# Kernel optimization log

Measured on AMD Instinct MI355X. Metric: run time of the kernel, lower is better.

The kernel has to match this reference:

```python
import jax, jax.numpy as jnp
import numpy as np

START, STOP, T = 28, 29, 30

def _lstm_dir(x, h0, c0, w_ih, w_hh, b_ih, b_hh):
    # x: (S, B, E) -> hs: (S, B, H)
    xw = jnp.einsum('sbe,ge->sbg', x, w_ih) + b_ih + b_hh  # (S,B,4H)
    def step(carry, g_x):
        h, c = carry
        g = g_x + h @ w_hh.T
        i, f, gg, o = jnp.split(g, 4, axis=-1)
        c = jax.nn.sigmoid(f) * c + jax.nn.sigmoid(i) * jnp.tanh(gg)
        h = jax.nn.sigmoid(o) * jnp.tanh(c)
        return (h, c), h
    _, hs = jax.lax.scan(step, (h0, c0), xw)
    return hs

def setup_inputs() -> dict:
    key = jax.random.key(0)
    ks = jax.random.split(key, 16)
    S, B, V, E, H = 256, 32, 50000, 512, 512  # H = hidden_dim // 2
    d = {}
    d['sentence'] = jax.random.randint(ks[0], (S, B), 0, V)
    d['tags'] = jax.random.randint(ks[1], (S, B), 0, 28)
    d['emb'] = jax.random.normal(ks[2], (V, E), jnp.float32) * 0.1
    d['w_ih_f'] = jax.random.normal(ks[3], (4 * H, E), jnp.float32) * 0.05
    d['w_hh_f'] = jax.random.normal(ks[4], (4 * H, H), jnp.float32) * 0.05
    d['b_ih_f'] = jax.random.normal(ks[5], (4 * H,), jnp.float32) * 0.05
    d['b_hh_f'] = jax.random.normal(ks[6], (4 * H,), jnp.float32) * 0.05
    d['w_ih_b'] = jax.random.normal(ks[7], (4 * H, E), jnp.float32) * 0.05
    d['w_hh_b'] = jax.random.normal(ks[8], (4 * H, H), jnp.float32) * 0.05
    d['b_ih_b'] = jax.random.normal(ks[9], (4 * H,), jnp.float32) * 0.05
    d['b_hh_b'] = jax.random.normal(ks[10], (4 * H,), jnp.float32) * 0.05
    d['w_out'] = jax.random.normal(ks[11], (T, 2 * H), jnp.float32) * 0.05
    d['b_out'] = jax.random.normal(ks[12], (T,), jnp.float32) * 0.05
    tr = jax.random.normal(ks[13], (T, T), jnp.float32)
    tr = tr.at[START, :].set(-10000.0).at[:, STOP].set(-10000.0)
    d['transitions'] = tr
    d['h0'] = jax.random.normal(ks[14], (2, B, H), jnp.float32)
    d['c0'] = jax.random.normal(ks[15], (2, B, H), jnp.float32)
    return d

def reference(sentence, tags, emb, w_ih_f, w_hh_f, b_ih_f, b_hh_f,
              w_ih_b, w_hh_b, b_ih_b, b_hh_b, w_out, b_out, transitions, h0, c0):
    S, B = sentence.shape
    x = emb[sentence]                                   # (S,B,E)
    hf = _lstm_dir(x, h0[0], c0[0], w_ih_f, w_hh_f, b_ih_f, b_hh_f)
    hb = _lstm_dir(x[::-1], h0[1], c0[1], w_ih_b, w_hh_b, b_ih_b, b_hh_b)[::-1]
    lstm_out = jnp.concatenate([hf, hb], axis=-1)       # (S,B,2H)
    feats = jnp.einsum('sbh,th->bst', lstm_out, w_out) + b_out  # (B,S,T)

    # CRF partition function (forward algorithm)
    fv0 = jnp.full((B, T), -10000.0, feats.dtype).at[:, START].set(0.0)
    def crf_step(fv, feat):  # fv (B,T), feat (B,T)
        fv = jax.nn.logsumexp(fv[:, None, :] + transitions[None, :, :] + feat[:, :, None], axis=2)
        return fv, None
    fv, _ = jax.lax.scan(crf_step, fv0, feats.transpose(1, 0, 2))
    forward_score = jax.nn.logsumexp(fv + transitions[STOP][None, :], axis=1)  # (B,)

    # gold path score
    tags_b = tags.T                                     # (B,S)
    tags_ext = jnp.concatenate([jnp.full((B, 1), START, tags_b.dtype), tags_b], axis=1)  # (B,S+1)
    t_prev, t_next = tags_ext[:, :-1], tags_ext[:, 1:]
    trans_sc = transitions[t_next, t_prev].sum(axis=1)
    emit_sc = jnp.take_along_axis(feats, t_next[:, :, None], axis=2)[:, :, 0].sum(axis=1)
    gold_score = trans_sc + emit_sc + transitions[STOP, tags_ext[:, -1]]

    return jnp.sum(forward_score - gold_score)
```

## Files before the change

### kernel.cpp

```cpp
#include <hip/hip_runtime.h>
#include <hip/hip_bf16.h>
#include <math.h>

#define S_LEN 256
#define B 32
#define E 512
#define H 512
#define G4 2048
#define T_TAGS 30
#define START_TAG 28
#define STOP_TAG 29

typedef unsigned short u16;
typedef unsigned int   u32;
typedef unsigned long long u64;
typedef __attribute__((ext_vector_type(8))) short bf16x8;
typedef __attribute__((ext_vector_type(4))) float f32x4;

__device__ __forceinline__ float bf2f(u16 u){
  u32 x = ((u32)u) << 16;
  return __uint_as_float(x);
}
__device__ __forceinline__ u16 f2bf(float f){
  u32 x = __float_as_uint(f);
  u32 r = (x + 0x7fffu + ((x >> 16) & 1u)) >> 16;
  return (u16)r;
}
__device__ __forceinline__ float sigf(float x){
  return 1.0f / (1.0f + __expf(-x));
}
__device__ __forceinline__ float tanh_fast(float x){
  return 1.0f - 2.0f / (__expf(2.0f * x) + 1.0f);
}

__global__ __launch_bounds__(256) void k_prep_a(
    const int* __restrict__ sent, const float* __restrict__ emb,
    u16* __restrict__ a16)
{
  int g = (blockIdx.x * 256 + threadIdx.x) * 8;
  int token = g >> 9, k = g & 511;
  const float* src = emb + (size_t)sent[token] * E + k;
  float4 v0 = *reinterpret_cast<const float4*>(src);
  float4 v1 = *reinterpret_cast<const float4*>(src + 4);
  u16 o[8];
  o[0]=f2bf(v0.x); o[1]=f2bf(v0.y); o[2]=f2bf(v0.z); o[3]=f2bf(v0.w);
  o[4]=f2bf(v1.x); o[5]=f2bf(v1.y); o[6]=f2bf(v1.z); o[7]=f2bf(v1.w);
  *reinterpret_cast<uint4*>(a16 + g) = *reinterpret_cast<const uint4*>(o);
}

__global__ __launch_bounds__(256) void k_cvt(const float* __restrict__ src, u16* __restrict__ dst){
  int g = (blockIdx.x * 256 + threadIdx.x) * 8;
  float4 v0 = *reinterpret_cast<const float4*>(src + g);
  float4 v1 = *reinterpret_cast<const float4*>(src + g + 4);
  u16 o[8];
  o[0]=f2bf(v0.x); o[1]=f2bf(v0.y); o[2]=f2bf(v0.z); o[3]=f2bf(v0.w);
  o[4]=f2bf(v1.x); o[5]=f2bf(v1.y); o[6]=f2bf(v1.z); o[7]=f2bf(v1.w);
  *reinterpret_cast<uint4*>(dst + g) = *reinterpret_cast<const uint4*>(o);
}

__global__ __launch_bounds__(256) void k_init16(
    const float* __restrict__ h0, u16* __restrict__ h16, u32* __restrict__ bar)
{
  int g = (blockIdx.x * 256 + threadIdx.x) * 8;
  float4 v0 = *reinterpret_cast<const float4*>(h0 + g);
  float4 v1 = *reinterpret_cast<const float4*>(h0 + g + 4);
  u16 o[8];
  o[0]=f2bf(v0.x); o[1]=f2bf(v0.y); o[2]=f2bf(v0.z); o[3]=f2bf(v0.w);
  o[4]=f2bf(v1.x); o[5]=f2bf(v1.y); o[6]=f2bf(v1.z); o[7]=f2bf(v1.w);
  *reinterpret_cast<uint4*>(h16 + g) = *reinterpret_cast<const uint4*>(o);
  if (blockIdx.x == 0 && threadIdx.x < 64) bar[threadIdx.x] = 0u;
}

__global__ __launch_bounds__(256) void k_gemm_xw16(
    const u16* __restrict__ a16, const u16* __restrict__ w16ih,
    const float* __restrict__ b_ih_f, const float* __restrict__ b_hh_f,
    const float* __restrict__ b_ih_b, const float* __restrict__ b_hh_b,
    u16* __restrict__ xw)
{
  int dir = blockIdx.z;
  int n0 = blockIdx.x * 128;
  int m0 = blockIdx.y * 128;
  const u16* Wp = w16ih + (size_t)dir * G4 * E;
  const float* bi = dir ? b_ih_b : b_ih_f;
  const float* bh = dir ? b_hh_b : b_hh_f;
  int tid = threadIdx.x;

  __shared__ u16 As[128 * 32];
  __shared__ u16 Bs[128 * 32];

  int l  = tid & 63;
  int wid = tid >> 6;
  int wr = wid >> 1, wc = wid & 1;
  int lr = l & 15, lh = l >> 4;
  int swzr = (lh ^ (lr & 3)) << 3;

  f32x4 acc[4][4];
  #pragma unroll
  for (int i = 0; i < 4; ++i)
    #pragma unroll
    for (int j = 0; j < 4; ++j)
      acc[i][j] = (f32x4){0.f, 0.f, 0.f, 0.f};

  for (int kt = 0; kt < E; kt += 32){
    __syncthreads();
    #pragma unroll
    for (int it = 0; it < 2; ++it){
      int u = it * 256 + tid;
      int row = u >> 2, c = u & 3;
      int sw = (c ^ (row & 3)) << 3;
      *reinterpret_cast<uint4*>(&As[row * 32 + sw]) =
        *reinterpret_cast<const uint4*>(a16 + (size_t)(m0 + row) * E + kt + c * 8);
      *reinterpret_cast<uint4*>(&Bs[row * 32 + sw]) =
        *reinterpret_cast<const uint4*>(Wp + (size_t)(n0 + row) * E + kt + c * 8);
    }
    __syncthreads();
    bf16x8 a[4], b[4];
    #pragma unroll
    for (int mi = 0; mi < 4; ++mi)
      a[mi] = *reinterpret_cast<const bf16x8*>(&As[(wr * 64 + mi * 16 + lr) * 32 + swzr]);
    #pragma unroll
    for (int ni = 0; ni < 4; ++ni)
      b[ni] = *reinterpret_cast<const bf16x8*>(&Bs[(wc * 64 + ni * 16 + lr) * 32 + swzr]);
    #pragma unroll
    for (int mi = 0; mi < 4; ++mi)
      #pragma unroll
      for (int ni = 0; ni < 4; ++ni)
        acc[mi][ni] = __builtin_amdgcn_mfma_f32_16x16x32_bf16(a[mi], b[ni], acc[mi][ni], 0, 0, 0);
  }

  #pragma unroll
  for (int ni = 0; ni < 4; ++ni){
    int n = n0 + wc * 64 + ni * 16 + lr;
    float bias = bi[n] + bh[n];
    #pragma unroll
    for (int mi = 0; mi < 4; ++mi){
      #pragma unroll
      for (int r = 0; r < 4; ++r){
        int m = m0 + wr * 64 + mi * 16 + lh * 4 + r;
        xw[((size_t)dir * 8192 + m) * G4 + n] = f2bf(acc[mi][ni][r] + bias);
      }
    }
  }
}

__global__ __launch_bounds__(256) void k_lstm_all(
    const u16* __restrict__ w16hh, const u16* __restrict__ xw,
    u16* __restrict__ h16,
    const float* __restrict__ c0,
    u16* __restrict__ hseq,
    u32* __restrict__ bar)
{
  __shared__ u16   w_s[64 * 512];
  __shared__ float gate_s[4][32][17];

  int bx    = blockIdx.x;
  int dir   = bx >> 5;
  int slice = bx & 31;
  int j0    = slice << 4;
  int tid   = threadIdx.x;

  #pragma unroll
  for (int i = 0; i < 16; ++i){
    int u = i * 256 + tid;
    int r = u >> 6, ku = u & 63;
    int g = r >> 4, jj = r & 15;
    const u16* src = w16hh + (size_t)dir * (G4 * H) + (size_t)((g << 9) + j0 + jj) * H + ku * 8;
    int idx = (r * 512 + ku * 8) ^ ((r & 7) << 3);
    *reinterpret_cast<uint4*>(&w_s[idx]) = *reinterpret_cast<const uint4*>(src);
  }

  int l  = tid & 63;
  int wid = tid >> 6;
  int wr = wid >> 1;
  int wc = wid & 1;
  int lr = l & 15, lh = l >> 4;

  int r0 = wc * 32 + lr;
  int r1 = r0 + 16;
  int base0 = r0 * 512 + lh * 8;
  int base1 = r1 * 512 + lh * 8;
  int sw = (lr & 7) << 3;

  int arow_u16 = ((wr << 4) + lr) * H + (lh << 3);

  int eb = tid >> 3;
  int ej = (tid & 7) << 1;
  float c_reg[2];
  c_reg[0] = c0[((size_t)dir * B + eb) * H + j0 + ej];
  c_reg[1] = c0[((size_t)dir * B + eb) * H + j0 + ej + 1];

  const u32* fl = bar + dir * 32;

  __syncthreads();

  for (int t = 0; t < S_LEN; ++t){
    int s_eff = dir ? (S_LEN - 1 - t) : t;

    const u16* xwp = xw + ((size_t)dir * 8192 + (size_t)s_eff * B + eb) * G4 + j0 + ej;
    u32 xi = *reinterpret_cast<const u32*>(xwp);
    u32 xf = *reinterpret_cast<const u32*>(xwp + 512);
    u32 xg = *reinterpret_cast<const u32*>(xwp + 1024);
    u32 xo = *reinterpret_cast<const u32*>(xwp + 1536);

    if (t > 0){
      if (tid < 32){
        while (__hip_atomic_load(fl + tid, __ATOMIC_RELAXED, __HIP_MEMORY_SCOPE_AGENT) < (u32)t)
          __builtin_amdgcn_s_sleep(1);
      }
      __syncthreads();
    }

    const u64* ap64 = reinterpret_cast<const u64*>(
        h16 + (size_t)(t & 1) * (2 * B * H) + (size_t)dir * (B * H) + arow_u16);
    u64 qa[32];
    #pragma unroll
    for (int kt = 0; kt < 16; ++kt){
      qa[2*kt]   = __hip_atomic_load(ap64 + kt * 8,     __ATOMIC_RELAXED, __HIP_MEMORY_SCOPE_AGENT);
      qa[2*kt+1] = __hip_atomic_load(ap64 + kt * 8 + 1, __ATOMIC_RELAXED, __HIP_MEMORY_SCOPE_AGENT);
    }

    f32x4 acc0 = {0.f,0.f,0.f,0.f}, acc1 = {0.f,0.f,0.f,0.f};
    #pragma unroll
    for (int kt = 0; kt < 16; ++kt){
      union { u64 q[2]; bf16x8 v; } ua;
      ua.q[0] = qa[2*kt]; ua.q[1] = qa[2*kt+1];
      bf16x8 b0 = *reinterpret_cast<const bf16x8*>(&w_s[(base0 + kt * 32) ^ sw]);
      bf16x8 b1 = *reinterpret_cast<const bf16x8*>(&w_s[(base1 + kt * 32) ^ sw]);
      acc0 = __builtin_amdgcn_mfma_f32_16x16x32_bf16(ua.v, b0, acc0, 0, 0, 0);
      acc1 = __builtin_amdgcn_mfma_f32_16x16x32_bf16(ua.v, b1, acc1, 0, 0, 0);
    }
    #pragma unroll
    for (int r = 0; r < 4; ++r){
      gate_s[wc * 2 + 0][(wr << 4) + (lh << 2) + r][lr] = acc0[r];
      gate_s[wc * 2 + 1][(wr << 4) + (lh << 2) + r][lr] = acc1[r];
    }
    __syncthreads();

    float hv[2];
    #pragma unroll
    for (int e = 0; e < 2; ++e){
      float iv = gate_s[0][eb][ej + e] + bf2f(e ? (u16)(xi >> 16) : (u16)(xi & 0xffff));
      float fv = gate_s[1][eb][ej + e] + bf2f(e ? (u16)(xf >> 16) : (u16)(xf & 0xffff));
      float gv = gate_s[2][eb][ej + e] + bf2f(e ? (u16)(xg >> 16) : (u16)(xg & 0xffff));
      float ov = gate_s[3][eb][ej + e] + bf2f(e ? (u16)(xo >> 16) : (u16)(xo & 0xffff));
      float cn = sigf(fv) * c_reg[e] + sigf(iv) * tanh_fast(gv);
      hv[e] = sigf(ov) * tanh_fast(cn);
      c_reg[e] = cn;
    }
    u32 hpack = (u32)f2bf(hv[0]) | ((u32)f2bf(hv[1]) << 16);
    size_t hoff = ((size_t)dir * B + eb) * H + j0 + ej;
    __hip_atomic_store(
        reinterpret_cast<u32*>(h16) + (((size_t)((t + 1) & 1) * (2 * B * H) + hoff) >> 1),
        hpack, __ATOMIC_RELAXED, __HIP_MEMORY_SCOPE_AGENT);
    *reinterpret_cast<u32*>(hseq + ((size_t)dir * 8192 + (size_t)s_eff * B + eb) * H + j0 + ej) = hpack;

    asm volatile("s_waitcnt vmcnt(0)" ::: "memory");
    __syncthreads();
    if (tid == 0)
      __hip_atomic_store(bar + dir * 32 + slice, (u32)(t + 1),
                         __ATOMIC_RELAXED, __HIP_MEMORY_SCOPE_AGENT);
  }
}

__global__ __launch_bounds__(256) void k_feats2(
    const u16* __restrict__ hseq, const float* __restrict__ w_out,
    const float* __restrict__ b_out, float* __restrict__ feats)
{
  __shared__ float row[32][1028];
  int blk = blockIdx.x;
  int tid = threadIdx.x;
  const u16* hf16 = hseq;
  const u16* hb16 = hseq + (size_t)8192 * H;

  #pragma unroll
  for (int it = 0; it < 16; ++it){
    int u = it * 256 + tid;
    int flat = u * 8;
    int i = flat >> 10, d = flat & 1023;
    int m = blk * 32 + i;
    const u16* src = (d < 512) ? (hf16 + (size_t)m * H + d) : (hb16 + (size_t)m * H + d - 512);
    uint4 v = *reinterpret_cast<const uint4*>(src);
    float* dst = &row[i][d];
    dst[0] = bf2f((u16)(v.x & 0xffff)); dst[1] = bf2f((u16)(v.x >> 16));
    dst[2] = bf2f((u16)(v.y & 0xffff)); dst[3] = bf2f((u16)(v.y >> 16));
    dst[4] = bf2f((u16)(v.z & 0xffff)); dst[5] = bf2f((u16)(v.z >> 16));
    dst[6] = bf2f((u16)(v.w & 0xffff)); dst[7] = bf2f((u16)(v.w >> 16));
  }
  __syncthreads();

  int i = tid >> 3, tg = tid & 7;
  const float* w0 = w_out + (size_t)((tg + 0  < T_TAGS) ? tg + 0  : 0) * 1024;
  const float* w1 = w_out + (size_t)((tg + 8  < T_TAGS) ? tg + 8  : 0) * 1024;
  const float* w2 = w_out + (size_t)((tg + 16 < T_TAGS) ? tg + 16 : 0) * 1024;
  const float* w3 = w_out + (size_t)((tg + 24 < T_TAGS) ? tg + 24 : 0) * 1024;
  float s0 = 0.f, s1 = 0.f, s2 = 0.f, s3 = 0.f;
  #pragma unroll 4
  for (int k4 = 0; k4 < 256; ++k4){
    float4 rv = *reinterpret_cast<const float4*>(&row[i][k4 * 4]);
    float4 a = *reinterpret_cast<const float4*>(w0 + k4 * 4);
    float4 b = *reinterpret_cast<const float4*>(w1 + k4 * 4);
    float4 c = *reinterpret_cast<const float4*>(w2 + k4 * 4);
    float4 d = *reinterpret_cast<const float4*>(w3 + k4 * 4);
    s0 = fmaf(a.x,rv.x,s0); s0 = fmaf(a.y,rv.y,s0); s0 = fmaf(a.z,rv.z,s0); s0 = fmaf(a.w,rv.w,s0);
    s1 = fmaf(b.x,rv.x,s1); s1 = fmaf(b.y,rv.y,s1); s1 = fmaf(b.z,rv.z,s1); s1 = fmaf(b.w,rv.w,s1);
    s2 = fmaf(c.x,rv.x,s2); s2 = fmaf(c.y,rv.y,s2); s2 = fmaf(c.z,rv.z,s2); s2 = fmaf(c.w,rv.w,s2);
    s3 = fmaf(d.x,rv.x,s3); s3 = fmaf(d.y,rv.y,s3); s3 = fmaf(d.z,rv.z,s3); s3 = fmaf(d.w,rv.w,s3);
  }
  int m = blk * 32 + i;
  int s = m >> 5, b = m & 31;
  float* fp = feats + ((size_t)b * S_LEN + s) * T_TAGS;
  float sums[4] = {s0, s1, s2, s3};
  #pragma unroll
  for (int q = 0; q < 4; ++q){
    int tt = tg + q * 8;
    if (tt < T_TAGS) fp[tt] = sums[q] + b_out[tt];
  }
}

__global__ __launch_bounds__(64) void k_crf2(
    const float* __restrict__ feats, const float* __restrict__ trans,
    const int* __restrict__ tags, float* __restrict__ scores)
{
  int b = blockIdx.x;
  int l = threadIdx.x;

  float trr[T_TAGS];
  #pragma unroll
  for (int j = 0; j < T_TAGS; ++j)
    trr[j] = (l < T_TAGS) ? trans[l * T_TAGS + j] : -1e30f;

  float fv = (l == START_TAG) ? 0.f : -10000.f;
  const float* fb = feats + (size_t)b * S_LEN * T_TAGS;

  for (int s = 0; s < S_LEN; ++s){
    float feat = (l < T_TAGS) ? fb[s * T_TAGS + l] : 0.f;
    float v[T_TAGS];
    float m = -1e30f;
    #pragma unroll
    for (int j = 0; j < T_TAGS; ++j){
      float fvj = __shfl(fv, j);
      v[j] = fvj + trr[j];
      m = fmaxf(m, v[j]);
    }
    float sum = 0.f;
    #pragma unroll
    for (int j = 0; j < T_TAGS; ++j) sum += __expf(v[j] - m);
    fv = feat + m + __logf(sum);
  }

  float fin = (l < T_TAGS) ? fv + trans[STOP_TAG * T_TAGS + l] : -1e30f;
  float mm = fin;
  #pragma unroll
  for (int o = 32; o > 0; o >>= 1) mm = fmaxf(mm, __shfl_xor(mm, o));
  float e = (l < T_TAGS) ? __expf(fin - mm) : 0.f;
  #pragma unroll
  for (int o = 32; o > 0; o >>= 1) e += __shfl_xor(e, o);
  float fsc = mm + __logf(e);

  float g = 0.f;
  #pragma unroll
  for (int it = 0; it < 4; ++it){
    int s = it * 64 + l;
    int nxt = tags[s * B + b];
    int prv = s ? tags[(s - 1) * B + b] : START_TAG;
    g += trans[nxt * T_TAGS + prv] + fb[s * T_TAGS + nxt];
  }
  #pragma unroll
  for (int o = 32; o > 0; o >>= 1) g += __shfl_down(g, o);
  if (l == 0){
    int last = tags[(S_LEN - 1) * B + b];
    g += trans[STOP_TAG * T_TAGS + last];
    scores[b] = fsc - g;
  }
}

__global__ void k_final(const float* __restrict__ scores, float* __restrict__ out){
  int tid = threadIdx.x;
  float v = (tid < B) ? scores[tid] : 0.f;
  #pragma unroll
  for (int o = 32; o > 0; o >>= 1) v += __shfl_down(v, o);
  if (tid == 0) out[0] = v;
}

extern "C" void kernel_launch(void* const* d_in, const int* in_sizes, int n_in,
                              void* d_out, int out_size, void* d_ws, size_t ws_size,
                              hipStream_t stream)
{
  const int*   sent   = (const int*)d_in[0];
  const int*   tags   = (const int*)d_in[1];
  const float* emb    = (const float*)d_in[2];
  const float* w_ih_f = (const float*)d_in[3];
  const float* w_hh_f = (const float*)d_in[4];
  const float* b_ih_f = (const float*)d_in[5];
  const float* b_hh_f = (const float*)d_in[6];
  const float* w_ih_b = (const float*)d_in[7];
  const float* w_hh_b = (const float*)d_in[8];
  const float* b_ih_b = (const float*)d_in[9];
  const float* b_hh_b = (const float*)d_in[10];
  const float* w_out  = (const float*)d_in[11];
  const float* b_out  = (const float*)d_in[12];
  const float* trans  = (const float*)d_in[13];
  const float* h0     = (const float*)d_in[14];
  const float* c0     = (const float*)d_in[15];

  const size_t OFF_XW   = 0;
  const size_t OFF_A16  = 67108864;
  const size_t OFF_WIH  = 75497472;
  const size_t OFF_WHH  = 79691776;
  const size_t OFF_HSEQ = 83886080;
  const size_t OFF_H16  = 100663296;
  const size_t OFF_FEATS= 100794368;
  const size_t OFF_SC   = 101777408;
  const size_t OFF_BAR  = 101777536;
  const size_t NEED     = 101777792;
  if (ws_size < NEED) return;

  char* ws = (char*)d_ws;
  u16*   xw     = (u16*)(ws + OFF_XW);
  u16*   a16    = (u16*)(ws + OFF_A16);
  u16*   w16ih  = (u16*)(ws + OFF_WIH);
  u16*   w16hh  = (u16*)(ws + OFF_WHH);
  u16*   hseq   = (u16*)(ws + OFF_HSEQ);
  u16*   h16    = (u16*)(ws + OFF_H16);
  float* feats  = (float*)(ws + OFF_FEATS);
  float* scores = (float*)(ws + OFF_SC);
  u32*   bar    = (u32*)(ws + OFF_BAR);

  k_prep_a<<<2048, 256, 0, stream>>>(sent, emb, a16);
  k_cvt<<<512, 256, 0, stream>>>(w_ih_f, w16ih);
  k_cvt<<<512, 256, 0, stream>>>(w_ih_b, w16ih + (size_t)G4 * E);
  k_cvt<<<512, 256, 0, stream>>>(w_hh_f, w16hh);
  k_cvt<<<512, 256, 0, stream>>>(w_hh_b, w16hh + (size_t)G4 * H);
  k_init16<<<16, 256, 0, stream>>>(h0, h16, bar);

  k_gemm_xw16<<<dim3(G4 / 128, 8192 / 128, 2), 256, 0, stream>>>(
      a16, w16ih, b_ih_f, b_hh_f, b_ih_b, b_hh_b, xw);

  k_lstm_all<<<64, 256, 0, stream>>>(w16hh, xw, h16, c0, hseq, bar);

  k_feats2<<<256, 256, 0, stream>>>(hseq, w_out, b_out, feats);
  k_crf2<<<B, 64, 0, stream>>>(feats, trans, tags, scores);
  k_final<<<1, 64, 0, stream>>>(scores, (float*)d_out);
}
```

Baseline: 1.859 ms.

## Replace per-block barrier flags with step-tagged hidden state words in LSTM recurrence

The recurrent kernel no longer uses a separate flag array and spin barrier. Each hidden value is now stored as a 32-bit word holding a bf16 value and the step counter, and readers poll the hidden-state words directly until every tag matches the current step. This removes the flag publish, the wait for the store to drain, and an extra syncthreads on the serial critical path. The MFMA work is also split along K across wave columns with a two-way reduction in shared memory, and the W_hh bf16 conversion is folded into the LSTM kernel's load, dropping two launches. The trade-off is twice the bytes per hidden-state read and a polling loop that may re-read the full operand set several times.

```diff
diff --git a/kernel.cpp b/kernel.cpp
--- a/kernel.cpp
+++ b/kernel.cpp
@@ -58,17 +58,22 @@
   *reinterpret_cast<uint4*>(dst + g) = *reinterpret_cast<const uint4*>(o);
 }
 
-__global__ __launch_bounds__(256) void k_init16(
-    const float* __restrict__ h0, u16* __restrict__ h16, u32* __restrict__ bar)
+__global__ __launch_bounds__(256) void k_init_ht(
+    const float* __restrict__ h0, u32* __restrict__ ht)
 {
   int g = (blockIdx.x * 256 + threadIdx.x) * 8;
   float4 v0 = *reinterpret_cast<const float4*>(h0 + g);
   float4 v1 = *reinterpret_cast<const float4*>(h0 + g + 4);
-  u16 o[8];
-  o[0]=f2bf(v0.x); o[1]=f2bf(v0.y); o[2]=f2bf(v0.z); o[3]=f2bf(v0.w);
-  o[4]=f2bf(v1.x); o[5]=f2bf(v1.y); o[6]=f2bf(v1.z); o[7]=f2bf(v1.w);
-  *reinterpret_cast<uint4*>(h16 + g) = *reinterpret_cast<const uint4*>(o);
-  if (blockIdx.x == 0 && threadIdx.x < 64) bar[threadIdx.x] = 0u;
+  u32 o[8];
+  o[0] = ((u32)f2bf(v0.x)) << 16; o[1] = ((u32)f2bf(v0.y)) << 16;
+  o[2] = ((u32)f2bf(v0.z)) << 16; o[3] = ((u32)f2bf(v0.w)) << 16;
+  o[4] = ((u32)f2bf(v1.x)) << 16; o[5] = ((u32)f2bf(v1.y)) << 16;
+  o[6] = ((u32)f2bf(v1.z)) << 16; o[7] = ((u32)f2bf(v1.w)) << 16;
+  #pragma unroll
+  for (int i = 0; i < 8; ++i){
+    ht[g + i] = o[i];
+    ht[32768 + g + i] = 0x0000ffffu;
+  }
 }
 
 __global__ __launch_bounds__(256) void k_gemm_xw16(
@@ -144,14 +149,14 @@
 }
 
 __global__ __launch_bounds__(256) void k_lstm_all(
-    const u16* __restrict__ w16hh, const u16* __restrict__ xw,
-    u16* __restrict__ h16,
+    const float* __restrict__ w_hh_f, const float* __restrict__ w_hh_b,
+    const u16* __restrict__ xw,
+    u32* __restrict__ ht,
     const float* __restrict__ c0,
-    u16* __restrict__ hseq,
-    u32* __restrict__ bar)
+    u16* __restrict__ hseq)
 {
   __shared__ u16   w_s[64 * 512];
-  __shared__ float gate_s[4][32][17];
+  __shared__ float gate_s[2][4][32][17];
 
   int bx    = blockIdx.x;
   int dir   = bx >> 5;
@@ -159,14 +164,20 @@
   int j0    = slice << 4;
   int tid   = threadIdx.x;
 
+  const float* wsrc = dir ? w_hh_b : w_hh_f;
   #pragma unroll
   for (int i = 0; i < 16; ++i){
     int u = i * 256 + tid;
-    int r = u >> 6, ku = u & 63;
+    int r = u >> 6, ku8 = u & 63;
     int g = r >> 4, jj = r & 15;
-    const u16* src = w16hh + (size_t)dir * (G4 * H) + (size_t)((g << 9) + j0 + jj) * H + ku * 8;
-    int idx = (r * 512 + ku * 8) ^ ((r & 7) << 3);
-    *reinterpret_cast<uint4*>(&w_s[idx]) = *reinterpret_cast<const uint4*>(src);
+    const float* src = wsrc + (size_t)((g << 9) + j0 + jj) * H + ku8 * 8;
+    float4 a = *reinterpret_cast<const float4*>(src);
+    float4 b = *reinterpret_cast<const float4*>(src + 4);
+    u16 o[8];
+    o[0]=f2bf(a.x); o[1]=f2bf(a.y); o[2]=f2bf(a.z); o[3]=f2bf(a.w);
+    o[4]=f2bf(b.x); o[5]=f2bf(b.y); o[6]=f2bf(b.z); o[7]=f2bf(b.w);
+    int idx = (r * 512 + ku8 * 8) ^ ((r & 7) << 3);
+    *reinterpret_cast<uint4*>(&w_s[idx]) = *reinterpret_cast<const uint4*>(o);
   }
 
   int l  = tid & 63;
@@ -174,22 +185,21 @@
   int wr = wid >> 1;
   int wc = wid & 1;
   int lr = l & 15, lh = l >> 4;
-
-  int r0 = wc * 32 + lr;
-  int r1 = r0 + 16;
-  int base0 = r0 * 512 + lh * 8;
-  int base1 = r1 * 512 + lh * 8;
   int sw = (lr & 7) << 3;
 
-  int arow_u16 = ((wr << 4) + lr) * H + (lh << 3);
+  int bbase[4];
+  #pragma unroll
+  for (int G = 0; G < 4; ++G)
+    bbase[G] = (G * 16 + lr) * 512 + (wc << 8) + (lh << 3);
+
+  int aoff = ((wr << 4) + lr) * 512 + (wc << 8) + (lh << 3);
 
   int eb = tid >> 3;
   int ej = (tid & 7) << 1;
-  float c_reg[2];
-  c_reg[0] = c0[((size_t)dir * B + eb) * H + j0 + ej];
-  c_reg[1] = c0[((size_t)dir * B + eb) * H + j0 + ej + 1];
-
-  const u32* fl = bar + dir * 32;
+  float c_reg0 = c0[((size_t)dir * B + eb) * H + j0 + ej];
+  float c_reg1 = c0[((size_t)dir * B + eb) * H + j0 + ej + 1];
+
+  const int PSTRIDE = 2 * B * H;
 
   __syncthreads();
 
@@ -202,63 +212,78 @@
     u32 xg = *reinterpret_cast<const u32*>(xwp + 1024);
     u32 xo = *reinterpret_cast<const u32*>(xwp + 1536);
 
-    if (t > 0){
-      if (tid < 32){
-        while (__hip_atomic_load(fl + tid, __ATOMIC_RELAXED, __HIP_MEMORY_SCOPE_AGENT) < (u32)t)
-          __builtin_amdgcn_s_sleep(1);
+    const u64* hp = reinterpret_cast<const u64*>(
+        ht + (size_t)(t & 1) * PSTRIDE + (size_t)dir * (B * H) + aoff);
+    u64 qa[32];
+    u64 tt = (u64)(u32)t | ((u64)(u32)t << 32);
+    for (;;){
+      #pragma unroll
+      for (int kt = 0; kt < 8; ++kt){
+        #pragma unroll
+        for (int q = 0; q < 4; ++q)
+          qa[kt * 4 + q] = __hip_atomic_load(hp + kt * 16 + q,
+                              __ATOMIC_RELAXED, __HIP_MEMORY_SCOPE_AGENT);
       }
-      __syncthreads();
-    }
-
-    const u64* ap64 = reinterpret_cast<const u64*>(
-        h16 + (size_t)(t & 1) * (2 * B * H) + (size_t)dir * (B * H) + arow_u16);
-    u64 qa[32];
-    #pragma unroll
-    for (int kt = 0; kt < 16; ++kt){
-      qa[2*kt]   = __hip_atomic_load(ap64 + kt * 8,     __ATOMIC_RELAXED, __HIP_MEMORY_SCOPE_AGENT);
-      qa[2*kt+1] = __hip_atomic_load(ap64 + kt * 8 + 1, __ATOMIC_RELAXED, __HIP_MEMORY_SCOPE_AGENT);
-    }
-
-    f32x4 acc0 = {0.f,0.f,0.f,0.f}, acc1 = {0.f,0.f,0.f,0.f};
-    #pragma unroll
-    for (int kt = 0; kt < 16; ++kt){
-      union { u64 q[2]; bf16x8 v; } ua;
-      ua.q[0] = qa[2*kt]; ua.q[1] = qa[2*kt+1];
-      bf16x8 b0 = *reinterpret_cast<const bf16x8*>(&w_s[(base0 + kt * 32) ^ sw]);
-      bf16x8 b1 = *reinterpret_cast<const bf16x8*>(&w_s[(base1 + kt * 32) ^ sw]);
-      acc0 = __builtin_amdgcn_mfma_f32_16x16x32_bf16(ua.v, b0, acc0, 0, 0, 0);
-      acc1 = __builtin_amdgcn_mfma_f32_16x16x32_bf16(ua.v, b1, acc1, 0, 0, 0);
-    }
-    #pragma unroll
-    for (int r = 0; r < 4; ++r){
-      gate_s[wc * 2 + 0][(wr << 4) + (lh << 2) + r][lr] = acc0[r];
-      gate_s[wc * 2 + 1][(wr << 4) + (lh << 2) + r][lr] = acc1[r];
-    }
+      u64 bad = 0;
+      #pragma unroll
+      for (int i2 = 0; i2 < 32; ++i2) bad |= (qa[i2] ^ tt);
+      if (!__any((bad & 0x0000ffff0000ffffull) != 0)) break;
+      __builtin_amdgcn_s_sleep(1);
+    }
+
+    f32x4 acc[4];
+    #pragma unroll
+    for (int G = 0; G < 4; ++G) acc[G] = (f32x4){0.f, 0.f, 0.f, 0.f};
+    #pragma unroll
+    for (int kt = 0; kt < 8; ++kt){
+      union { u32 w[4]; bf16x8 v; } af;
+      #pragma unroll
+      for (int q = 0; q < 4; ++q)
+        af.w[q] = __builtin_amdgcn_perm((u32)(qa[kt * 4 + q] >> 32),
+                                        (u32)(qa[kt * 4 + q]), 0x07060302u);
+      #pragma unroll
+      for (int G = 0; G < 4; ++G){
+        bf16x8 bfr = *reinterpret_cast<const bf16x8*>(&w_s[(bbase[G] + (kt << 5)) ^ sw]);
+        acc[G] = __builtin_amdgcn_mfma_f32_16x16x32_bf16(af.v, bfr, acc[G], 0, 0, 0);
+      }
+    }
+    #pragma unroll
+    for (int G = 0; G < 4; ++G)
+      #pragma unroll
+      for (int r = 0; r < 4; ++r)
+        gate_s[wc][G][(wr << 4) + (lh << 2) + r][lr] = acc[G][r];
     __syncthreads();
 
-    float hv[2];
-    #pragma unroll
-    for (int e = 0; e < 2; ++e){
-      float iv = gate_s[0][eb][ej + e] + bf2f(e ? (u16)(xi >> 16) : (u16)(xi & 0xffff));
-      float fv = gate_s[1][eb][ej + e] + bf2f(e ? (u16)(xf >> 16) : (u16)(xf & 0xffff));
-      float gv = gate_s[2][eb][ej + e] + bf2f(e ? (u16)(xg >> 16) : (u16)(xg & 0xffff));
-      float ov = gate_s[3][eb][ej + e] + bf2f(e ? (u16)(xo >> 16) : (u16)(xo & 0xffff));
-      float cn = sigf(fv) * c_reg[e] + sigf(iv) * tanh_fast(gv);
-      hv[e] = sigf(ov) * tanh_fast(cn);
-      c_reg[e] = cn;
-    }
-    u32 hpack = (u32)f2bf(hv[0]) | ((u32)f2bf(hv[1]) << 16);
-    size_t hoff = ((size_t)dir * B + eb) * H + j0 + ej;
-    __hip_atomic_store(
-        reinterpret_cast<u32*>(h16) + (((size_t)((t + 1) & 1) * (2 * B * H) + hoff) >> 1),
-        hpack, __ATOMIC_RELAXED, __HIP_MEMORY_SCOPE_AGENT);
-    *reinterpret_cast<u32*>(hseq + ((size_t)dir * 8192 + (size_t)s_eff * B + eb) * H + j0 + ej) = hpack;
-
-    asm volatile("s_waitcnt vmcnt(0)" ::: "memory");
+    float hv0, hv1;
+    {
+      float iv = gate_s[0][0][eb][ej] + gate_s[1][0][eb][ej] + bf2f((u16)(xi & 0xffff));
+      float fv = gate_s[0][1][eb][ej] + gate_s[1][1][eb][ej] + bf2f((u16)(xf & 0xffff));
+      float gv = gate_s[0][2][eb][ej] + gate_s[1][2][eb][ej] + bf2f((u16)(xg & 0xffff));
+      float ov = gate_s[0][3][eb][ej] + gate_s[1][3][eb][ej] + bf2f((u16)(xo & 0xffff));
+      float cn = sigf(fv) * c_reg0 + sigf(iv) * tanh_fast(gv);
+      hv0 = sigf(ov) * tanh_fast(cn);
+      c_reg0 = cn;
+    }
+    {
+      float iv = gate_s[0][0][eb][ej+1] + gate_s[1][0][eb][ej+1] + bf2f((u16)(xi >> 16));
+      float fv = gate_s[0][1][eb][ej+1] + gate_s[1][1][eb][ej+1] + bf2f((u16)(xf >> 16));
+      float gv = gate_s[0][2][eb][ej+1] + gate_s[1][2][eb][ej+1] + bf2f((u16)(xg >> 16));
+      float ov = gate_s[0][3][eb][ej+1] + gate_s[1][3][eb][ej+1] + bf2f((u16)(xo >> 16));
+      float cn = sigf(fv) * c_reg1 + sigf(iv) * tanh_fast(gv);
+      hv1 = sigf(ov) * tanh_fast(cn);
+      c_reg1 = cn;
+    }
+    u16 h0b = f2bf(hv0), h1b = f2bf(hv1);
+    u32 w0 = ((u32)h0b << 16) | (u32)(t + 1);
+    u32 w1 = ((u32)h1b << 16) | (u32)(t + 1);
+    size_t hoff = (size_t)((t + 1) & 1) * PSTRIDE + ((size_t)dir * B + eb) * H + j0 + ej;
+    __hip_atomic_store(reinterpret_cast<u64*>(ht + hoff),
+                       (u64)w0 | ((u64)w1 << 32),
+                       __ATOMIC_RELAXED, __HIP_MEMORY_SCOPE_AGENT);
+    *reinterpret_cast<u32*>(hseq + ((size_t)dir * 8192 + (size_t)s_eff * B + eb) * H + j0 + ej) =
+        (u32)h0b | ((u32)h1b << 16);
+
     __syncthreads();
-    if (tid == 0)
-      __hip_atomic_store(bar + dir * 32 + slice, (u32)(t + 1),
-                         __ATOMIC_RELAXED, __HIP_MEMORY_SCOPE_AGENT);
   }
 }
 
@@ -406,37 +431,31 @@
   const size_t OFF_XW   = 0;
   const size_t OFF_A16  = 67108864;
   const size_t OFF_WIH  = 75497472;
-  const size_t OFF_WHH  = 79691776;
-  const size_t OFF_HSEQ = 83886080;
-  const size_t OFF_H16  = 100663296;
-  const size_t OFF_FEATS= 100794368;
-  const size_t OFF_SC   = 101777408;
-  const size_t OFF_BAR  = 101777536;
-  const size_t NEED     = 101777792;
+  const size_t OFF_HSEQ = 79691776;
+  const size_t OFF_HT   = 96468992;
+  const size_t OFF_FEATS= 96731136;
+  const size_t OFF_SC   = 97714176;
+  const size_t NEED     = 97714304;
   if (ws_size < NEED) return;
 
   char* ws = (char*)d_ws;
   u16*   xw     = (u16*)(ws + OFF_XW);
   u16*   a16    = (u16*)(ws + OFF_A16);
   u16*   w16ih  = (u16*)(ws + OFF_WIH);
-  u16*   w16hh  = (u16*)(ws + OFF_WHH);
   u16*   hseq   = (u16*)(ws + OFF_HSEQ);
-  u16*   h16    = (u16*)(ws + OFF_H16);
+  u32*   ht     = (u32*)(ws + OFF_HT);
   float* feats  = (float*)(ws + OFF_FEATS);
   float* scores = (float*)(ws + OFF_SC);
-  u32*   bar    = (u32*)(ws + OFF_BAR);
 
   k_prep_a<<<2048, 256, 0, stream>>>(sent, emb, a16);
   k_cvt<<<512, 256, 0, stream>>>(w_ih_f, w16ih);
   k_cvt<<<512, 256, 0, stream>>>(w_ih_b, w16ih + (size_t)G4 * E);
-  k_cvt<<<512, 256, 0, stream>>>(w_hh_f, w16hh);
-  k_cvt<<<512, 256, 0, stream>>>(w_hh_b, w16hh + (size_t)G4 * H);
-  k_init16<<<16, 256, 0, stream>>>(h0, h16, bar);
+  k_init_ht<<<16, 256, 0, stream>>>(h0, ht);
 
   k_gemm_xw16<<<dim3(G4 / 128, 8192 / 128, 2), 256, 0, stream>>>(
       a16, w16ih, b_ih_f, b_hh_f, b_ih_b, b_hh_b, xw);
 
-  k_lstm_all<<<64, 256, 0, stream>>>(w16hh, xw, h16, c0, hseq, bar);
+  k_lstm_all<<<64, 256, 0, stream>>>(w_hh_f, w_hh_b, xw, ht, c0, hseq);
 
   k_feats2<<<256, 256, 0, stream>>>(hseq, w_out, b_out, feats);
   k_crf2<<<B, 64, 0, stream>>>(feats, trans, tags, scores);
```

Measured after the change: 2.182 ms. 1.17x slower.
